# Kernel optimization log

Hardware: AMD Instinct MI355X
Metric: run time of the kernel (lower is better)

## Reference

```python
import jax, jax.numpy as jnp
import numpy as np


def setup_inputs() -> dict:
    key = jax.random.key(0)
    # Uniform in (0.9, 1.1) so the running product over 8192 elements stays finite.
    x = jax.random.uniform(key, (4096, 8192), dtype=jnp.float32, minval=0.9, maxval=1.1)
    return {"x": x}


def reference(x) -> jnp.ndarray:
    # Inclusive prefix product along dim 1 (matches cumprod_dim1_cuda / torch.cumprod(x, dim=1)).
    return jnp.cumprod(x, axis=1)
```

## Files before the change

kernel.cpp:

```cpp
#include <hip/hip_runtime.h>


#define N    8192
#define T    256
#define NW   (T / 64)
#define SEG  (N / NW)
#define QV   (SEG / 256)

typedef float f32x4 __attribute__((ext_vector_type(4)));

__device__ __forceinline__ float readlane63(float x) {
    return __builtin_bit_cast(float,
        __builtin_amdgcn_readlane(__builtin_bit_cast(int, x), 63));
}

template<int CTRL, int RM, int BM>
__device__ __forceinline__ float dpp_id1(float x) {
    int r = __builtin_amdgcn_update_dpp(
        __builtin_bit_cast(int, 1.0f), __builtin_bit_cast(int, x),
        CTRL, RM, BM, false);
    return __builtin_bit_cast(float, r);
}

__device__ __forceinline__ float wave_scan_mul(float x) {
    x *= dpp_id1<0x111, 0xf, 0xf>(x);
    x *= dpp_id1<0x112, 0xf, 0xf>(x);
    x *= dpp_id1<0x114, 0xf, 0xf>(x);
    x *= dpp_id1<0x118, 0xf, 0xf>(x);
    x *= dpp_id1<0x142, 0xa, 0xf>(x);
    x *= dpp_id1<0x143, 0xc, 0xf>(x);
    return x;
}

__global__ __launch_bounds__(T) void cumprod_rows_kernel(
    const float* __restrict__ x, float* __restrict__ out, int n_rows)
{
    __shared__ float wsum[NW];

    const int row = blockIdx.x;
    if (row >= n_rows) return;
    const int tid  = threadIdx.x;
    const int lane = tid & 63;
    const int wid  = tid >> 6;

    const size_t base = (size_t)row * N + (size_t)wid * SEG;
    const float* __restrict__ xr   = x   + base;
    float*       __restrict__ outr = out + base;

    f32x4 d[QV];
#pragma unroll
    for (int v = 0; v < QV; ++v)
        d[v] = *reinterpret_cast<const f32x4*>(xr + v * 256 + lane * 4);

    float t[QV];
#pragma unroll
    for (int v = 0; v < QV; ++v) {
        d[v].y *= d[v].x;
        d[v].z *= d[v].y;
        d[v].w *= d[v].z;
        t[v] = d[v].w;
    }

    float ep[QV];
#pragma unroll
    for (int v = 0; v < QV; ++v) {
        const float e = __shfl_up(t[v], 1, 64);
        ep[v] = (lane == 0) ? 1.0f : e;
    }

    float carry = 1.0f;
    float coef[QV];
#pragma unroll
    for (int v = 0; v < QV; ++v) {
        const float exc = wave_scan_mul(ep[v]);
        coef[v] = carry * exc;
        carry  *= readlane63(exc * t[v]);
    }

    if (lane == 0) wsum[wid] = carry;
    __syncthreads();

    float wpre = 1.0f;
#pragma unroll
    for (int w = 0; w < NW - 1; ++w)
        if (w < wid) wpre *= wsum[w];

#pragma unroll
    for (int v = 0; v < QV; ++v) {
        const float f = wpre * coef[v];
        f32x4 o = d[v];
        o.x *= f; o.y *= f; o.z *= f; o.w *= f;
        __builtin_nontemporal_store(
            o, reinterpret_cast<f32x4*>(outr + v * 256 + lane * 4));
    }
}

extern "C" void kernel_launch(void* const* d_in, const int* in_sizes, int n_in,
                              void* d_out, int out_size, void* d_ws, size_t ws_size,
                              hipStream_t stream)
{
    const float* x   = (const float*)d_in[0];
    float*       out = (float*)d_out;
    const int n_rows = in_sizes[0] / N;
    cumprod_rows_kernel<<<n_rows, T, 0, stream>>>(x, out, n_rows);
}
```

Measured before the change: 232.7 us.

## Split row cumprod into segment-reduce and seeded-scan kernels for more parallelism

Replaces the one-block-per-row scan with a reduce-then-scan scheme: a first kernel computes each 1024-element segment's product into workspace, and a second kernel rescans each segment seeded by the product of its preceding segments. This raises the number of independent waves and lowers per-wave register footprint to improve latency hiding. In exchange it reads the input twice and adds a second launch, and falls back to the old single-pass kernel when no workspace is provided.

```diff
diff --git a/kernel.cpp b/kernel.cpp
--- a/kernel.cpp
+++ b/kernel.cpp
@@ -2,10 +2,11 @@
 
 
 #define N    8192
+#define SEG  1024
+#define SPR  (N / SEG)
+#define QV   (SEG / 256)
 #define T    256
-#define NW   (T / 64)
-#define SEG  (N / NW)
-#define QV   (SEG / 256)
+#define WPB  (T / 64)
 
 typedef float f32x4 __attribute__((ext_vector_type(4)));
 
@@ -32,61 +33,121 @@
     return x;
 }
 
-__global__ __launch_bounds__(T) void cumprod_rows_kernel(
+__global__ __launch_bounds__(T) void seed_kernel(
+    const float* __restrict__ x, float* __restrict__ seeds, int n_rows)
+{
+    const int gw   = blockIdx.x * WPB + (threadIdx.x >> 6);
+    const int lane = threadIdx.x & 63;
+    const int row  = gw / SPR;
+    const int seg  = gw % SPR;
+    if (row >= n_rows) return;
+
+    const float* __restrict__ xr = x + (size_t)row * N + (size_t)seg * SEG;
+
+    f32x4 d[QV];
+#pragma unroll
+    for (int v = 0; v < QV; ++v)
+        d[v] = *reinterpret_cast<const f32x4*>(xr + (v * 64 + lane) * 4);
+
+    float q[QV];
+#pragma unroll
+    for (int v = 0; v < QV; ++v)
+        q[v] = (d[v].x * d[v].y) * (d[v].z * d[v].w);
+    const float p = (q[0] * q[1]) * (q[2] * q[3]);
+
+    const float inc = wave_scan_mul(p);
+    if (lane == 63) seeds[(size_t)row * SPR + seg] = inc;
+}
+
+__global__ __launch_bounds__(T) void scan_kernel(
+    const float* __restrict__ x, const float* __restrict__ seeds,
+    float* __restrict__ out, int n_rows)
+{
+    const int gw   = blockIdx.x * WPB + (threadIdx.x >> 6);
+    const int lane = threadIdx.x & 63;
+    const int row  = gw / SPR;
+    const int seg  = gw % SPR;
+    if (row >= n_rows) return;
+
+    const size_t base = (size_t)row * N + (size_t)seg * SEG;
+
+    f32x4 d[QV];
+#pragma unroll
+    for (int v = 0; v < QV; ++v)
+        d[v] = *reinterpret_cast<const f32x4*>(x + base + (v * 64 + lane) * 4);
+
+    const float* __restrict__ sr = seeds + (size_t)row * SPR;
+    const f32x4 s0 = *reinterpret_cast<const f32x4*>(sr);
+    const f32x4 s1 = *reinterpret_cast<const f32x4*>(sr + 4);
+    float spre = 1.0f;
+    spre *= (seg > 0) ? s0.x : 1.0f;
+    spre *= (seg > 1) ? s0.y : 1.0f;
+    spre *= (seg > 2) ? s0.z : 1.0f;
+    spre *= (seg > 3) ? s0.w : 1.0f;
+    spre *= (seg > 4) ? s1.x : 1.0f;
+    spre *= (seg > 5) ? s1.y : 1.0f;
+    spre *= (seg > 6) ? s1.z : 1.0f;
+
+    float carry = spre;
+    float coef[QV];
+#pragma unroll
+    for (int v = 0; v < QV; ++v) {
+        d[v].y *= d[v].x;
+        d[v].z *= d[v].y;
+        d[v].w *= d[v].z;
+        const float t = d[v].w;
+        const float e = __shfl_up(t, 1, 64);
+        const float ep = (lane == 0) ? 1.0f : e;
+        const float exc = wave_scan_mul(ep);
+        coef[v] = carry * exc;
+        carry  *= readlane63(exc * t);
+    }
+
+#pragma unroll
+    for (int v = 0; v < QV; ++v) {
+        f32x4 o = d[v];
+        o.x *= coef[v]; o.y *= coef[v]; o.z *= coef[v]; o.w *= coef[v];
+        __builtin_nontemporal_store(
+            o, reinterpret_cast<f32x4*>(out + base + (v * 64 + lane) * 4));
+    }
+}
+
+__global__ __launch_bounds__(T) void cumprod_rows_fallback(
     const float* __restrict__ x, float* __restrict__ out, int n_rows)
 {
-    __shared__ float wsum[NW];
-
+    __shared__ float wsum[WPB];
     const int row = blockIdx.x;
     if (row >= n_rows) return;
     const int tid  = threadIdx.x;
     const int lane = tid & 63;
     const int wid  = tid >> 6;
-
-    const size_t base = (size_t)row * N + (size_t)wid * SEG;
+    const size_t base = (size_t)row * N + (size_t)wid * (N / WPB);
     const float* __restrict__ xr   = x   + base;
     float*       __restrict__ outr = out + base;
 
-    f32x4 d[QV];
+    f32x4 d[8];
 #pragma unroll
-    for (int v = 0; v < QV; ++v)
+    for (int v = 0; v < 8; ++v)
         d[v] = *reinterpret_cast<const f32x4*>(xr + v * 256 + lane * 4);
-
-    float t[QV];
+    float carry = 1.0f, coef[8];
 #pragma unroll
-    for (int v = 0; v < QV; ++v) {
-        d[v].y *= d[v].x;
-        d[v].z *= d[v].y;
-        d[v].w *= d[v].z;
-        t[v] = d[v].w;
+    for (int v = 0; v < 8; ++v) {
+        d[v].y *= d[v].x; d[v].z *= d[v].y; d[v].w *= d[v].z;
+        const float t = d[v].w;
+        const float e = __shfl_up(t, 1, 64);
+        const float ep = (lane == 0) ? 1.0f : e;
+        const float exc = wave_scan_mul(ep);
+        coef[v] = carry * exc;
+        carry  *= readlane63(exc * t);
     }
-
-    float ep[QV];
-#pragma unroll
-    for (int v = 0; v < QV; ++v) {
-        const float e = __shfl_up(t[v], 1, 64);
-        ep[v] = (lane == 0) ? 1.0f : e;
-    }
-
-    float carry = 1.0f;
-    float coef[QV];
-#pragma unroll
-    for (int v = 0; v < QV; ++v) {
-        const float exc = wave_scan_mul(ep[v]);
-        coef[v] = carry * exc;
-        carry  *= readlane63(exc * t[v]);
-    }
-
     if (lane == 0) wsum[wid] = carry;
     __syncthreads();
-
     float wpre = 1.0f;
 #pragma unroll
-    for (int w = 0; w < NW - 1; ++w)
+    for (int w = 0; w < WPB - 1; ++w)
         if (w < wid) wpre *= wsum[w];
-
 #pragma unroll
-    for (int v = 0; v < QV; ++v) {
+    for (int v = 0; v < 8; ++v) {
         const float f = wpre * coef[v];
         f32x4 o = d[v];
         o.x *= f; o.y *= f; o.z *= f; o.w *= f;
@@ -102,5 +163,14 @@
     const float* x   = (const float*)d_in[0];
     float*       out = (float*)d_out;
     const int n_rows = in_sizes[0] / N;
-    cumprod_rows_kernel<<<n_rows, T, 0, stream>>>(x, out, n_rows);
+    const size_t seed_bytes = (size_t)n_rows * SPR * sizeof(float);
+
+    if (d_ws != nullptr && ws_size >= seed_bytes) {
+        float* seeds = (float*)d_ws;
+        const int nblk = (n_rows * SPR) / WPB;
+        seed_kernel<<<nblk, T, 0, stream>>>(x, seeds, n_rows);
+        scan_kernel<<<nblk, T, 0, stream>>>(x, seeds, out, n_rows);
+    } else {
+        cumprod_rows_fallback<<<n_rows, T, 0, stream>>>(x, out, n_rows);
+    }
 }
```

Result: slower. 241.6 us (+3.8%).

## Scan one row per wave with double-buffered global-to-LDS tile streaming

Applied to the files above, without the earlier changes.

Each row moves from a whole 256-thread block to a single wave, so the cross-wave shared-memory exchange and __syncthreads go away. The wave walks its row in 1024-element tiles with a running carry. The next tile is prefetched into a double-buffered LDS area with direct global_load_lds while the current tile is scanned and stored, with manual vmcnt waits between the two. The cost is 32KB of LDS per block, which may limit occupancy, plus a serial carry chain along the whole row inside each wave.

```diff
diff --git a/kernel.cpp b/kernel.cpp
--- a/kernel.cpp
+++ b/kernel.cpp
@@ -1,13 +1,16 @@
 #include <hip/hip_runtime.h>
 
 
-#define N    8192
-#define T    256
-#define NW   (T / 64)
-#define SEG  (N / NW)
-#define QV   (SEG / 256)
+#define N     8192
+#define T     256
+#define WPB   (T / 64)
+#define TILE  1024
+#define NT    (N / TILE)
+#define CHK   (TILE / 256)
 
 typedef float f32x4 __attribute__((ext_vector_type(4)));
+typedef const __attribute__((address_space(1))) float glb_f;
+typedef __attribute__((address_space(3))) float lds_f;
 
 __device__ __forceinline__ float readlane63(float x) {
     return __builtin_bit_cast(float,
@@ -35,63 +38,67 @@
 __global__ __launch_bounds__(T) void cumprod_rows_kernel(
     const float* __restrict__ x, float* __restrict__ out, int n_rows)
 {
-    __shared__ float wsum[NW];
+    __shared__ float lds[WPB][2][TILE];
 
-    const int row = blockIdx.x;
+    const int lane = threadIdx.x & 63;
+    const int wid  = threadIdx.x >> 6;
+    const int row  = blockIdx.x * WPB + wid;
     if (row >= n_rows) return;
-    const int tid  = threadIdx.x;
-    const int lane = tid & 63;
-    const int wid  = tid >> 6;
 
-    const size_t base = (size_t)row * N + (size_t)wid * SEG;
-    const float* __restrict__ xr   = x   + base;
-    float*       __restrict__ outr = out + base;
+    const float* __restrict__ xr   = x   + (size_t)row * N;
+    float*       __restrict__ outr = out + (size_t)row * N;
 
-    f32x4 d[QV];
 #pragma unroll
-    for (int v = 0; v < QV; ++v)
-        d[v] = *reinterpret_cast<const f32x4*>(xr + v * 256 + lane * 4);
-
-    float t[QV];
-#pragma unroll
-    for (int v = 0; v < QV; ++v) {
-        d[v].y *= d[v].x;
-        d[v].z *= d[v].y;
-        d[v].w *= d[v].z;
-        t[v] = d[v].w;
-    }
-
-    float ep[QV];
-#pragma unroll
-    for (int v = 0; v < QV; ++v) {
-        const float e = __shfl_up(t[v], 1, 64);
-        ep[v] = (lane == 0) ? 1.0f : e;
-    }
+    for (int c = 0; c < CHK; ++c)
+        __builtin_amdgcn_global_load_lds(
+            (glb_f*)(xr + c * 256 + lane * 4),
+            (lds_f*)&lds[wid][0][c * 256], 16, 0, 0);
 
     float carry = 1.0f;
-    float coef[QV];
-#pragma unroll
-    for (int v = 0; v < QV; ++v) {
-        const float exc = wave_scan_mul(ep[v]);
-        coef[v] = carry * exc;
-        carry  *= readlane63(exc * t[v]);
-    }
-
-    if (lane == 0) wsum[wid] = carry;
-    __syncthreads();
-
-    float wpre = 1.0f;
-#pragma unroll
-    for (int w = 0; w < NW - 1; ++w)
-        if (w < wid) wpre *= wsum[w];
 
 #pragma unroll
-    for (int v = 0; v < QV; ++v) {
-        const float f = wpre * coef[v];
-        f32x4 o = d[v];
-        o.x *= f; o.y *= f; o.z *= f; o.w *= f;
-        __builtin_nontemporal_store(
-            o, reinterpret_cast<f32x4*>(outr + v * 256 + lane * 4));
+    for (int t = 0; t < NT; ++t) {
+        const int b = t & 1;
+
+        if (t + 1 < NT) {
+#pragma unroll
+            for (int c = 0; c < CHK; ++c)
+                __builtin_amdgcn_global_load_lds(
+                    (glb_f*)(xr + (t + 1) * TILE + c * 256 + lane * 4),
+                    (lds_f*)&lds[wid][b ^ 1][c * 256], 16, 0, 0);
+        }
+
+        if (t == 0 || t == NT - 1)
+            asm volatile("s_waitcnt vmcnt(4)" ::: "memory");
+        else
+            asm volatile("s_waitcnt vmcnt(8)" ::: "memory");
+        __builtin_amdgcn_sched_barrier(0);
+
+        f32x4 d[CHK];
+        float coef[CHK];
+#pragma unroll
+        for (int c = 0; c < CHK; ++c) {
+            d[c] = *reinterpret_cast<const f32x4*>(
+                       &lds[wid][b][c * 256 + lane * 4]);
+            d[c].y *= d[c].x;
+            d[c].z *= d[c].y;
+            d[c].w *= d[c].z;
+            const float tt = d[c].w;
+            const float e  = __shfl_up(tt, 1, 64);
+            const float ep = (lane == 0) ? 1.0f : e;
+            const float exc = wave_scan_mul(ep);
+            coef[c] = carry * exc;
+            carry  *= readlane63(exc * tt);
+        }
+
+#pragma unroll
+        for (int c = 0; c < CHK; ++c) {
+            f32x4 o = d[c];
+            o.x *= coef[c]; o.y *= coef[c];
+            o.z *= coef[c]; o.w *= coef[c];
+            __builtin_nontemporal_store(
+                o, reinterpret_cast<f32x4*>(outr + t * TILE + c * 256 + lane * 4));
+        }
     }
 }
 
@@ -102,5 +109,6 @@
     const float* x   = (const float*)d_in[0];
     float*       out = (float*)d_out;
     const int n_rows = in_sizes[0] / N;
-    cumprod_rows_kernel<<<n_rows, T, 0, stream>>>(x, out, n_rows);
+    const int nblk   = (n_rows + WPB - 1) / WPB;
+    cumprod_rows_kernel<<<nblk, T, 0, stream>>>(x, out, n_rows);
 }
```

After: 228.5 us. No clear change (-1.8%).
